# Kernel tuning notes

Measured on AMD Instinct MI355X. Metric: run time of the kernel, lower is better.

## Reference

```python
import jax, jax.numpy as jnp
import numpy as np

N = 100000
E = 1600000
IN_DIM = 128
HID = 64
HEADS = 4
OUT_DIM = 2
BN_EPS = 1e-5
NEG_SLOPE = 0.2


def setup_inputs() -> dict:
    key = jax.random.key(0)
    ks = jax.random.split(key, 16)
    inp = {
        "x": jax.random.normal(ks[0], (N, IN_DIM), jnp.float32),
        "edge_index": jax.random.randint(ks[1], (2, E), 0, N, jnp.int32),
        # layer 1: GATConv(IN_DIM, HID, heads=HEADS, concat=True)
        "W1": jax.random.normal(ks[2], (IN_DIM, HEADS * HID), jnp.float32) * 0.05,
        "att_src1": jax.random.normal(ks[3], (HEADS, HID), jnp.float32) * 0.05,
        "att_dst1": jax.random.normal(ks[4], (HEADS, HID), jnp.float32) * 0.05,
        "b1": jnp.zeros((HEADS * HID,), jnp.float32),
        # BatchNorm1d(HEADS*HID), eval mode (running stats)
        "gamma": jnp.ones((HEADS * HID,), jnp.float32),
        "beta": jnp.zeros((HEADS * HID,), jnp.float32),
        "rmean": jax.random.normal(ks[5], (HEADS * HID,), jnp.float32) * 0.01,
        "rvar": jnp.ones((HEADS * HID,), jnp.float32),
        # layer 2: GATConv(HEADS*HID, OUT_DIM, heads=1, concat=False)
        "W2": jax.random.normal(ks[6], (HEADS * HID, OUT_DIM), jnp.float32) * 0.05,
        "att_src2": jax.random.normal(ks[7], (1, OUT_DIM), jnp.float32) * 0.05,
        "att_dst2": jax.random.normal(ks[8], (1, OUT_DIM), jnp.float32) * 0.05,
        "b2": jnp.zeros((OUT_DIM,), jnp.float32),
    }
    return inp


def gat_conv(x, W, att_src, att_dst, src, dst):
    """PyG-style GATConv message passing. Returns [N, H, C] aggregated output."""
    H, C = att_src.shape
    h = (x @ W).reshape(-1, H, C)                      # [N,H,C]
    a_src = jnp.einsum('nhc,hc->nh', h, att_src)       # [N,H]
    a_dst = jnp.einsum('nhc,hc->nh', h, att_dst)       # [N,H]
    e = jax.nn.leaky_relu(a_src[src] + a_dst[dst], NEG_SLOPE)   # [E,H]
    # softmax over incoming edges per destination node (segment softmax)
    m = jax.ops.segment_max(e, dst, num_segments=h.shape[0])    # [N,H]
    ee = jnp.exp(e - m[dst])
    s = jax.ops.segment_sum(ee, dst, num_segments=h.shape[0])   # [N,H]
    alpha = ee / (s[dst] + 1e-16)                      # [E,H]
    msg = h[src] * alpha[:, :, None]                   # [E,H,C]
    return jax.ops.segment_sum(msg, dst, num_segments=h.shape[0])  # [N,H,C]


def reference(x, edge_index, W1, att_src1, att_dst1, b1,
              gamma, beta, rmean, rvar, W2, att_src2, att_dst2, b2):
    src, dst = edge_index[0], edge_index[1]
    # layer 1 (concat heads) + bias
    h = gat_conv(x, W1, att_src1, att_dst1, src, dst).reshape(N, HEADS * HID) + b1
    # BatchNorm1d (eval mode), ELU; dropout is identity in eval
    h = (h - rmean) * jax.lax.rsqrt(rvar + BN_EPS) * gamma + beta
    h = jax.nn.elu(h)
    # layer 2 (heads=1, concat=False -> mean over heads == squeeze) + bias
    out = gat_conv(h, W2, att_src2, att_dst2, src, dst).reshape(N, OUT_DIM) + b2
    return jax.nn.log_softmax(out, axis=1)
```

## Files before the change

kernel.cpp:

```cpp
#include <hip/hip_runtime.h>
#include <hip/hip_fp16.h>
#include <math.h>

#define NN 100000
#define EE 1600000
#define NEG 0.2f
#define NB 98
#define STRIP 128
#define GB 782
#define HB 6250

typedef _Float16 fh8 __attribute__((ext_vector_type(8)));
typedef float f32x4 __attribute__((ext_vector_type(4)));

__device__ __forceinline__ float lrelu(float v) { return v > 0.f ? v : NEG * v; }

__device__ __forceinline__ void fma8(const uint4& r, float w, float* acc)
{
    float2 f0 = __half22float2(*(const __half2*)&r.x);
    float2 f1 = __half22float2(*(const __half2*)&r.y);
    float2 f2 = __half22float2(*(const __half2*)&r.z);
    float2 f3 = __half22float2(*(const __half2*)&r.w);
    acc[0] = fmaf(w, f0.x, acc[0]); acc[1] = fmaf(w, f0.y, acc[1]);
    acc[2] = fmaf(w, f1.x, acc[2]); acc[3] = fmaf(w, f1.y, acc[3]);
    acc[4] = fmaf(w, f2.x, acc[4]); acc[5] = fmaf(w, f2.y, acc[5]);
    acc[6] = fmaf(w, f3.x, acc[6]); acc[7] = fmaf(w, f3.y, acc[7]);
}

__global__ __launch_bounds__(256) void prep_kernel(
    const float* __restrict__ W1,
    const float* __restrict__ b1, const float* __restrict__ gamma,
    const float* __restrict__ beta, const float* __restrict__ rmean,
    const float* __restrict__ rvar,
    _Float16* __restrict__ W1f, float* __restrict__ nA, float* __restrict__ nB,
    int* __restrict__ counts)
{
    int t = blockIdx.x * 256 + threadIdx.x;
    if (t < 64 * 64) {
        int l = t & 63, frag = t >> 6;
        int kk = frag & 3, ft = (frag >> 2) & 3, w = frag >> 4;
        int feat = w * 64 + ft * 16 + (l & 15);
        int kbase = kk * 32 + (l >> 4) * 8;
        _Float16 v[8];
#pragma unroll
        for (int i = 0; i < 8; i++) v[i] = (_Float16)W1[(size_t)(kbase + i) * 256 + feat];
        *(fh8*)&W1f[(size_t)t * 8] = *(fh8*)v;
    } else if (t < 64 * 64 + 256) {
        int f = t - 64 * 64;
        float scale = gamma[f] * rsqrtf(rvar[f] + 1e-5f);
        nA[f] = scale;
        nB[f] = (b1[f] - rmean[f]) * scale + beta[f];
    }
    for (int i = t; i < NN; i += 128 * 256) counts[i] = 0;
}

__global__ __launch_bounds__(256) void gemm1_hist(
    const float* __restrict__ x, const _Float16* __restrict__ W1f,
    const float* __restrict__ attS1, const float* __restrict__ attD1,
    __half* __restrict__ h1, float* __restrict__ asrc1, float* __restrict__ adst1,
    const int* __restrict__ ei, int* __restrict__ counts)
{
    const int bid = blockIdx.x;
    const int tid = threadIdx.x;
    if (bid >= GB) {
        int e = (bid - GB) * 256 + tid;
        if (e < EE) atomicAdd(&counts[ei[EE + e]], 1);
        return;
    }

    __shared__ _Float16 xh[STRIP][136];
    const int lane = tid & 63;
    const int w    = tid >> 6;
    const int base = bid * STRIP;

#pragma unroll
    for (int it = 0; it < 2; ++it) {
        int slot = tid + it * 256;
        int node = slot >> 2;
        int k0   = (slot & 3) * 32;
        int gnode = base + node;
        float4 buf[8];
        if (gnode < NN) {
            const float4* src = (const float4*)(x + (size_t)gnode * 128 + k0);
#pragma unroll
            for (int j = 0; j < 8; j++) buf[j] = src[j];
        } else {
#pragma unroll
            for (int j = 0; j < 8; j++) buf[j] = make_float4(0.f, 0.f, 0.f, 0.f);
        }
        _Float16* dst = &xh[node][k0];
#pragma unroll
        for (int j = 0; j < 8; j++) {
            dst[j * 4 + 0] = (_Float16)buf[j].x;
            dst[j * 4 + 1] = (_Float16)buf[j].y;
            dst[j * 4 + 2] = (_Float16)buf[j].z;
            dst[j * 4 + 3] = (_Float16)buf[j].w;
        }
    }
    __syncthreads();

    fh8 afrag[4][4];
    const fh8* wf = (const fh8*)W1f;
#pragma unroll
    for (int ft = 0; ft < 4; ft++)
#pragma unroll
        for (int kk = 0; kk < 4; kk++)
            afrag[ft][kk] = wf[((w * 4 + ft) * 4 + kk) * 64 + lane];

    const int nrow = lane & 15;
    const int kq   = lane >> 4;

    float attSv[4][4], attDv[4][4];
#pragma unroll
    for (int ft = 0; ft < 4; ft++)
#pragma unroll
        for (int r = 0; r < 4; r++) {
            int feat = w * 64 + ft * 16 + kq * 4 + r;
            attSv[ft][r] = attS1[feat];
            attDv[ft][r] = attD1[feat];
        }

    for (int g = 0; g < STRIP / 16; ++g) {
        fh8 b[4];
#pragma unroll
        for (int kk = 0; kk < 4; kk++)
            b[kk] = *(const fh8*)&xh[g * 16 + nrow][kk * 32 + kq * 8];

        f32x4 d[4];
#pragma unroll
        for (int ft = 0; ft < 4; ft++) {
            d[ft] = (f32x4){0.f, 0.f, 0.f, 0.f};
#pragma unroll
            for (int kk = 0; kk < 4; kk++)
                d[ft] = __builtin_amdgcn_mfma_f32_16x16x32_f16(afrag[ft][kk], b[kk], d[ft], 0, 0, 0);
        }

        int gnode = base + g * 16 + nrow;
        if (gnode < NN) {
            float ps = 0.f, pd = 0.f;
#pragma unroll
            for (int ft = 0; ft < 4; ft++) {
                __half hb[4];
#pragma unroll
                for (int r = 0; r < 4; r++) {
                    float v = d[ft][r];
                    hb[r] = __float2half(v);
                    ps = fmaf(v, attSv[ft][r], ps);
                    pd = fmaf(v, attDv[ft][r], pd);
                }
                *(float2*)&h1[(size_t)gnode * 256 + w * 64 + ft * 16 + kq * 4] = *(float2*)hb;
            }
            ps += __shfl_xor(ps, 16); ps += __shfl_xor(ps, 32);
            pd += __shfl_xor(pd, 16); pd += __shfl_xor(pd, 32);
            if (kq == 0) { asrc1[gnode * 4 + w] = ps; adst1[gnode * 4 + w] = pd; }
        }
    }
}

__global__ __launch_bounds__(256) void scan1_kernel(const int* __restrict__ counts, int* __restrict__ bsum)
{
    __shared__ int red[256];
    int t = threadIdx.x;
    int i0 = blockIdx.x * 1024 + t * 4;
    int s = 0;
    if (i0 + 3 < NN) {
        int4 v = *(const int4*)&counts[i0];
        s = v.x + v.y + v.z + v.w;
    } else {
#pragma unroll
        for (int j = 0; j < 4; j++) { int i = i0 + j; if (i < NN) s += counts[i]; }
    }
    red[t] = s;
    __syncthreads();
    for (int off = 128; off > 0; off >>= 1) {
        if (t < off) red[t] += red[t + off];
        __syncthreads();
    }
    if (t == 0) bsum[blockIdx.x] = red[0];
}

__global__ void scan2_kernel(const int* __restrict__ bsum, int* __restrict__ bbase, int* __restrict__ offs)
{
    __shared__ int sh[128];
    int t = threadIdx.x;
    int v = (t < NB) ? bsum[t] : 0;
    sh[t] = v;
    __syncthreads();
    for (int off = 1; off < 128; off <<= 1) {
        int u = (t >= off) ? sh[t - off] : 0;
        __syncthreads();
        sh[t] += u;
        __syncthreads();
    }
    if (t < NB) bbase[t] = sh[t] - v;
    if (t == 0) offs[NN] = EE;
}

__global__ __launch_bounds__(256) void scan3_kernel(const int* __restrict__ counts,
                                                    const int* __restrict__ bbase,
                                                    int* __restrict__ offs, int* __restrict__ cursor)
{
    __shared__ int sh[256];
    int t = threadIdx.x;
    int i0 = blockIdx.x * 1024 + t * 4;
    int c[4];
    int s = 0;
#pragma unroll
    for (int j = 0; j < 4; j++) { int i = i0 + j; c[j] = (i < NN) ? counts[i] : 0; s += c[j]; }
    sh[t] = s;
    __syncthreads();
    for (int off = 1; off < 256; off <<= 1) {
        int u = (t >= off) ? sh[t - off] : 0;
        __syncthreads();
        sh[t] += u;
        __syncthreads();
    }
    int run = bbase[blockIdx.x] + sh[t] - s;
    if (i0 + 3 < NN) {
        int4 o;
        o.x = run; run += c[0];
        o.y = run; run += c[1];
        o.z = run; run += c[2];
        o.w = run;
        *(int4*)&offs[i0] = o;
        *(int4*)&cursor[i0] = o;
    } else {
#pragma unroll
        for (int j = 0; j < 4; j++) { int i = i0 + j; if (i < NN) { offs[i] = run; cursor[i] = run; run += c[j]; } }
    }
}

__global__ void scatter_kernel(const int* __restrict__ ei,
                               const float* __restrict__ asrc1, const float* __restrict__ adst1,
                               int* __restrict__ cursor, int* __restrict__ csr_src,
                               float* __restrict__ ewp)
{
    int e = blockIdx.x * 256 + threadIdx.x;
    if (e >= EE) return;
    int s = ei[e], d = ei[EE + e];
    int pos = atomicAdd(&cursor[d], 1);
    csr_src[pos] = s;
    float4 as = *(const float4*)&asrc1[(size_t)s * 4];
    float4 ad = *(const float4*)&adst1[(size_t)d * 4];
    float4 w;
    w.x = expf(lrelu(as.x + ad.x));
    w.y = expf(lrelu(as.y + ad.y));
    w.z = expf(lrelu(as.z + ad.z));
    w.w = expf(lrelu(as.w + ad.w));
    *(float4*)&ewp[(size_t)pos * 4] = w;
}

__global__ __launch_bounds__(256) void agg1_kernel(
    const int* __restrict__ offs, const int* __restrict__ csr_src,
    const float* __restrict__ ewp, const __half* __restrict__ h1,
    float* __restrict__ g1)
{
    int wid  = (blockIdx.x * 256 + threadIdx.x) >> 6;
    int lane = threadIdx.x & 63;
    if (wid >= NN) return;
    int lo = offs[wid], hi = offs[wid + 1];
    const int ep   = lane >> 5;
    const int fl   = lane & 31;
    const int head = fl >> 3;

    float acc[8] = {0.f, 0.f, 0.f, 0.f, 0.f, 0.f, 0.f, 0.f};
    float wsum = 0.f;

    int base = lo;
    for (; base + 3 < hi; base += 4) {
        int idx0 = base + ep;
        int idx1 = base + 2 + ep;
        int s0 = csr_src[idx0];
        int s1 = csr_src[idx1];
        float w0 = ewp[(size_t)idx0 * 4 + head];
        float w1 = ewp[(size_t)idx1 * 4 + head];
        uint4 r0 = *(const uint4*)(h1 + (size_t)s0 * 256 + fl * 8);
        uint4 r1 = *(const uint4*)(h1 + (size_t)s1 * 256 + fl * 8);
        fma8(r0, w0, acc);
        fma8(r1, w1, acc);
        wsum += w0 + w1;
    }
    for (; base < hi; base += 2) {
        int idx = base + ep;
        float w = 0.f;
        uint4 r = make_uint4(0, 0, 0, 0);
        if (idx < hi) {
            int s = csr_src[idx];
            w = ewp[(size_t)idx * 4 + head];
            r = *(const uint4*)(h1 + (size_t)s * 256 + fl * 8);
        }
        fma8(r, w, acc);
        wsum += w;
    }

#pragma unroll
    for (int j = 0; j < 8; j++) acc[j] += __shfl_xor(acc[j], 32);
    wsum += __shfl_xor(wsum, 32);

    if (lane < 32) {
        float inv = 1.f / (wsum + 1e-16f);
        *(float4*)&g1[(size_t)wid * 256 + fl * 8]     = make_float4(acc[0] * inv, acc[1] * inv, acc[2] * inv, acc[3] * inv);
        *(float4*)&g1[(size_t)wid * 256 + fl * 8 + 4] = make_float4(acc[4] * inv, acc[5] * inv, acc[6] * inv, acc[7] * inv);
    }
}

__global__ __launch_bounds__(256) void node2_kernel(
    const float* __restrict__ g1,
    const float* __restrict__ nA, const float* __restrict__ nB,
    const float* __restrict__ W2, const float* __restrict__ attS2, const float* __restrict__ attD2,
    float4* __restrict__ pk2)
{
    int n    = blockIdx.x * 4 + (threadIdx.x >> 6);
    int lane = threadIdx.x & 63;
    if (n >= NN) return;
    int f4 = lane * 4;
    float4 v  = *(const float4*)&g1[(size_t)n * 256 + f4];
    float4 na = *(const float4*)&nA[f4];
    float4 nb = *(const float4*)&nB[f4];
    float va[4] = {v.x, v.y, v.z, v.w};
    float naa[4] = {na.x, na.y, na.z, na.w};
    float nba[4] = {nb.x, nb.y, nb.z, nb.w};
    float t[4];
#pragma unroll
    for (int j = 0; j < 4; j++) {
        float u = fmaf(va[j], naa[j], nba[j]);
        t[j] = u > 0.f ? u : expm1f(u);
    }
    float4 w01 = *(const float4*)&W2[(size_t)f4 * 2];
    float4 w23 = *(const float4*)&W2[(size_t)f4 * 2 + 4];
    float c0 = t[0] * w01.x + t[1] * w01.z + t[2] * w23.x + t[3] * w23.z;
    float c1 = t[0] * w01.y + t[1] * w01.w + t[2] * w23.y + t[3] * w23.w;
    for (int off = 1; off < 64; off <<= 1) {
        c0 += __shfl_xor(c0, off);
        c1 += __shfl_xor(c1, off);
    }
    if (lane == 0) {
        float as2 = c0 * attS2[0] + c1 * attS2[1];
        float ad2 = c0 * attD2[0] + c1 * attD2[1];
        pk2[n] = make_float4(as2, ad2, c0, c1);
    }
}

__global__ __launch_bounds__(256) void agg2_kernel(
    const int* __restrict__ offs, const int* __restrict__ csr_src,
    const float4* __restrict__ pk2, const float* __restrict__ b2,
    float* __restrict__ out)
{
    int wid  = (blockIdx.x * 256 + threadIdx.x) >> 6;
    int lane = threadIdx.x & 63;
    int grp  = lane >> 3;
    int sub  = lane & 7;
    int n = wid * 8 + grp;
    if (n >= NN) return;
    int lo = offs[n], hi = offs[n + 1];
    float ad = pk2[n].y;

    float n0 = 0.f, n1 = 0.f, ws = 0.f;
    for (int i = lo + sub; i < hi; i += 8) {
        int s = csr_src[i];
        float4 p = pk2[s];
        float w = expf(lrelu(p.x + ad));
        n0 = fmaf(w, p.z, n0);
        n1 = fmaf(w, p.w, n1);
        ws += w;
    }
    n0 += __shfl_xor(n0, 1); n0 += __shfl_xor(n0, 2); n0 += __shfl_xor(n0, 4);
    n1 += __shfl_xor(n1, 1); n1 += __shfl_xor(n1, 2); n1 += __shfl_xor(n1, 4);
    ws += __shfl_xor(ws, 1); ws += __shfl_xor(ws, 2); ws += __shfl_xor(ws, 4);

    if (sub == 0) {
        float inv = 1.f / (ws + 1e-16f);
        float v0 = n0 * inv + b2[0];
        float v1 = n1 * inv + b2[1];
        float m = fmaxf(v0, v1);
        float lse = m + log1pf(expf(fminf(v0, v1) - m));
        *(float2*)&out[(size_t)n * 2] = make_float2(v0 - lse, v1 - lse);
    }
}

extern "C" void kernel_launch(void* const* d_in, const int* in_sizes, int n_in,
                              void* d_out, int out_size, void* d_ws, size_t ws_size,
                              hipStream_t stream)
{
    const float* x     = (const float*)d_in[0];
    const int*   ei    = (const int*)d_in[1];
    const float* W1    = (const float*)d_in[2];
    const float* attS1 = (const float*)d_in[3];
    const float* attD1 = (const float*)d_in[4];
    const float* b1    = (const float*)d_in[5];
    const float* gamma = (const float*)d_in[6];
    const float* beta  = (const float*)d_in[7];
    const float* rmean = (const float*)d_in[8];
    const float* rvar  = (const float*)d_in[9];
    const float* W2    = (const float*)d_in[10];
    const float* attS2 = (const float*)d_in[11];
    const float* attD2 = (const float*)d_in[12];
    const float* b2    = (const float*)d_in[13];
    float* out = (float*)d_out;

    float* f = (float*)d_ws;
    __half* h1    = (__half*)f;
    float* asrc1  = f + (size_t)NN * 128;
    float* adst1  = asrc1 + (size_t)NN * 4;
    _Float16* W1f = (_Float16*)(adst1 + (size_t)NN * 4);
    float* nA     = adst1 + (size_t)NN * 4 + 16384;
    float* nB     = nA + 256;
    float4* pk2   = (float4*)(nB + 256);
    float* g1     = nB + 256 + (size_t)NN * 4;
    float* ewp    = g1 + (size_t)NN * 256;
    int* counts   = (int*)(ewp + (size_t)EE * 4);
    int* offs     = counts + NN;
    int* cursor   = offs + (NN + 1);
    int* bsum     = cursor + NN;
    int* bbase    = bsum + NB;
    int* csr_src  = bbase + NB;

    prep_kernel<<<128, 256, 0, stream>>>(W1, b1, gamma, beta, rmean, rvar, W1f, nA, nB, counts);

    gemm1_hist<<<GB + HB, 256, 0, stream>>>(x, W1f, attS1, attD1, h1, asrc1, adst1, ei, counts);

    scan1_kernel<<<NB, 256, 0, stream>>>(counts, bsum);
    scan2_kernel<<<1, 128, 0, stream>>>(bsum, bbase, offs);
    scan3_kernel<<<NB, 256, 0, stream>>>(counts, bbase, offs, cursor);

    scatter_kernel<<<HB, 256, 0, stream>>>(ei, asrc1, adst1, cursor, csr_src, ewp);

    agg1_kernel<<<(NN + 3) / 4, 256, 0, stream>>>(offs, csr_src, ewp, h1, g1);

    node2_kernel<<<(NN + 3) / 4, 256, 0, stream>>>(g1, nA, nB, W2, attS2, attD2, pk2);

    agg2_kernel<<<(NN + 31) / 32, 256, 0, stream>>>(offs, csr_src, pk2, b2, out);
}
```

Measured before the change: 344.5 us.

## Fuse node2 into agg1 and pack CSR source with fp16 edge weights

The layer-1 aggregation now feeds the BatchNorm, ELU and W2 projection straight from registers, so the 100000x256 float g1 buffer is never written and read back and one kernel launch goes away. The CSR source index and the four per-head exp weights are packed into a single 16-byte int4 record, with the weights stored as fp16, replacing separate csr_src and fp32 ewp arrays. This is meant to cut scatter and gather traffic. In exchange, edge weights lose precision, agg2 reads 16-byte records where it only needs the 4-byte index, and lanes 32-63 now do duplicate epilogue work.

```diff
diff --git a/kernel.cpp b/kernel.cpp
--- a/kernel.cpp
+++ b/kernel.cpp
@@ -25,6 +25,13 @@
     acc[2] = fmaf(w, f1.x, acc[2]); acc[3] = fmaf(w, f1.y, acc[3]);
     acc[4] = fmaf(w, f2.x, acc[4]); acc[5] = fmaf(w, f2.y, acc[5]);
     acc[6] = fmaf(w, f3.x, acc[6]); acc[7] = fmaf(w, f3.y, acc[7]);
+}
+
+__device__ __forceinline__ float ewgt(const int4& e, int head)
+{
+    uint p = (head < 2) ? (uint)e.y : (uint)e.z;
+    float2 f = __half22float2(*(const __half2*)&p);
+    return (head & 1) ? f.y : f.x;
 }
 
 __global__ __launch_bounds__(256) void prep_kernel(
@@ -232,28 +239,30 @@
 
 __global__ void scatter_kernel(const int* __restrict__ ei,
                                const float* __restrict__ asrc1, const float* __restrict__ adst1,
-                               int* __restrict__ cursor, int* __restrict__ csr_src,
-                               float* __restrict__ ewp)
+                               int* __restrict__ cursor, int4* __restrict__ csr)
 {
     int e = blockIdx.x * 256 + threadIdx.x;
     if (e >= EE) return;
     int s = ei[e], d = ei[EE + e];
     int pos = atomicAdd(&cursor[d], 1);
-    csr_src[pos] = s;
     float4 as = *(const float4*)&asrc1[(size_t)s * 4];
     float4 ad = *(const float4*)&adst1[(size_t)d * 4];
-    float4 w;
-    w.x = expf(lrelu(as.x + ad.x));
-    w.y = expf(lrelu(as.y + ad.y));
-    w.z = expf(lrelu(as.z + ad.z));
-    w.w = expf(lrelu(as.w + ad.w));
-    *(float4*)&ewp[(size_t)pos * 4] = w;
-}
-
-__global__ __launch_bounds__(256) void agg1_kernel(
-    const int* __restrict__ offs, const int* __restrict__ csr_src,
-    const float* __restrict__ ewp, const __half* __restrict__ h1,
-    float* __restrict__ g1)
+    __half2 w01 = __floats2half2_rn(expf(lrelu(as.x + ad.x)), expf(lrelu(as.y + ad.y)));
+    __half2 w23 = __floats2half2_rn(expf(lrelu(as.z + ad.z)), expf(lrelu(as.w + ad.w)));
+    int4 ent;
+    ent.x = s;
+    ent.y = *(const int*)&w01;
+    ent.z = *(const int*)&w23;
+    ent.w = 0;
+    csr[pos] = ent;
+}
+
+__global__ __launch_bounds__(256) void agg1_node2(
+    const int* __restrict__ offs, const int4* __restrict__ csr,
+    const __half* __restrict__ h1,
+    const float* __restrict__ nA, const float* __restrict__ nB,
+    const float* __restrict__ W2, const float* __restrict__ attS2, const float* __restrict__ attD2,
+    float4* __restrict__ pk2)
 {
     int wid  = (blockIdx.x * 256 + threadIdx.x) >> 6;
     int lane = threadIdx.x & 63;
@@ -270,12 +279,12 @@
     for (; base + 3 < hi; base += 4) {
         int idx0 = base + ep;
         int idx1 = base + 2 + ep;
-        int s0 = csr_src[idx0];
-        int s1 = csr_src[idx1];
-        float w0 = ewp[(size_t)idx0 * 4 + head];
-        float w1 = ewp[(size_t)idx1 * 4 + head];
-        uint4 r0 = *(const uint4*)(h1 + (size_t)s0 * 256 + fl * 8);
-        uint4 r1 = *(const uint4*)(h1 + (size_t)s1 * 256 + fl * 8);
+        int4 e0 = csr[idx0];
+        int4 e1 = csr[idx1];
+        float w0 = ewgt(e0, head);
+        float w1 = ewgt(e1, head);
+        uint4 r0 = *(const uint4*)(h1 + (size_t)e0.x * 256 + fl * 8);
+        uint4 r1 = *(const uint4*)(h1 + (size_t)e1.x * 256 + fl * 8);
         fma8(r0, w0, acc);
         fma8(r1, w1, acc);
         wsum += w0 + w1;
@@ -285,9 +294,9 @@
         float w = 0.f;
         uint4 r = make_uint4(0, 0, 0, 0);
         if (idx < hi) {
-            int s = csr_src[idx];
-            w = ewp[(size_t)idx * 4 + head];
-            r = *(const uint4*)(h1 + (size_t)s * 256 + fl * 8);
+            int4 e = csr[idx];
+            w = ewgt(e, head);
+            r = *(const uint4*)(h1 + (size_t)e.x * 256 + fl * 8);
         }
         fma8(r, w, acc);
         wsum += w;
@@ -297,52 +306,39 @@
     for (int j = 0; j < 8; j++) acc[j] += __shfl_xor(acc[j], 32);
     wsum += __shfl_xor(wsum, 32);
 
-    if (lane < 32) {
-        float inv = 1.f / (wsum + 1e-16f);
-        *(float4*)&g1[(size_t)wid * 256 + fl * 8]     = make_float4(acc[0] * inv, acc[1] * inv, acc[2] * inv, acc[3] * inv);
-        *(float4*)&g1[(size_t)wid * 256 + fl * 8 + 4] = make_float4(acc[4] * inv, acc[5] * inv, acc[6] * inv, acc[7] * inv);
-    }
-}
-
-__global__ __launch_bounds__(256) void node2_kernel(
-    const float* __restrict__ g1,
-    const float* __restrict__ nA, const float* __restrict__ nB,
-    const float* __restrict__ W2, const float* __restrict__ attS2, const float* __restrict__ attD2,
-    float4* __restrict__ pk2)
-{
-    int n    = blockIdx.x * 4 + (threadIdx.x >> 6);
-    int lane = threadIdx.x & 63;
-    if (n >= NN) return;
-    int f4 = lane * 4;
-    float4 v  = *(const float4*)&g1[(size_t)n * 256 + f4];
-    float4 na = *(const float4*)&nA[f4];
-    float4 nb = *(const float4*)&nB[f4];
-    float va[4] = {v.x, v.y, v.z, v.w};
-    float naa[4] = {na.x, na.y, na.z, na.w};
-    float nba[4] = {nb.x, nb.y, nb.z, nb.w};
-    float t[4];
-#pragma unroll
-    for (int j = 0; j < 4; j++) {
-        float u = fmaf(va[j], naa[j], nba[j]);
-        t[j] = u > 0.f ? u : expm1f(u);
-    }
-    float4 w01 = *(const float4*)&W2[(size_t)f4 * 2];
-    float4 w23 = *(const float4*)&W2[(size_t)f4 * 2 + 4];
-    float c0 = t[0] * w01.x + t[1] * w01.z + t[2] * w23.x + t[3] * w23.z;
-    float c1 = t[0] * w01.y + t[1] * w01.w + t[2] * w23.y + t[3] * w23.w;
-    for (int off = 1; off < 64; off <<= 1) {
-        c0 += __shfl_xor(c0, off);
-        c1 += __shfl_xor(c1, off);
-    }
+    float inv = 1.f / (wsum + 1e-16f);
+
+    float c0 = 0.f, c1 = 0.f;
+#pragma unroll
+    for (int half8 = 0; half8 < 2; ++half8) {
+        float4 na = *(const float4*)&nA[fl * 8 + half8 * 4];
+        float4 nb = *(const float4*)&nB[fl * 8 + half8 * 4];
+        float naa[4] = {na.x, na.y, na.z, na.w};
+        float nba[4] = {nb.x, nb.y, nb.z, nb.w};
+#pragma unroll
+        for (int j = 0; j < 4; j++) {
+            int f = fl * 8 + half8 * 4 + j;
+            float g = acc[half8 * 4 + j] * inv;
+            float u = fmaf(g, naa[j], nba[j]);
+            float t = u > 0.f ? u : expm1f(u);
+            c0 = fmaf(t, W2[f * 2],     c0);
+            c1 = fmaf(t, W2[f * 2 + 1], c1);
+        }
+    }
+    c0 += __shfl_xor(c0, 1); c0 += __shfl_xor(c0, 2); c0 += __shfl_xor(c0, 4);
+    c0 += __shfl_xor(c0, 8); c0 += __shfl_xor(c0, 16);
+    c1 += __shfl_xor(c1, 1); c1 += __shfl_xor(c1, 2); c1 += __shfl_xor(c1, 4);
+    c1 += __shfl_xor(c1, 8); c1 += __shfl_xor(c1, 16);
+
     if (lane == 0) {
         float as2 = c0 * attS2[0] + c1 * attS2[1];
         float ad2 = c0 * attD2[0] + c1 * attD2[1];
-        pk2[n] = make_float4(as2, ad2, c0, c1);
+        pk2[wid] = make_float4(as2, ad2, c0, c1);
     }
 }
 
 __global__ __launch_bounds__(256) void agg2_kernel(
-    const int* __restrict__ offs, const int* __restrict__ csr_src,
+    const int* __restrict__ offs, const int4* __restrict__ csr,
     const float4* __restrict__ pk2, const float* __restrict__ b2,
     float* __restrict__ out)
 {
@@ -357,7 +353,7 @@
 
     float n0 = 0.f, n1 = 0.f, ws = 0.f;
     for (int i = lo + sub; i < hi; i += 8) {
-        int s = csr_src[i];
+        int s = csr[i].x;
         float4 p = pk2[s];
         float w = expf(lrelu(p.x + ad));
         n0 = fmaf(w, p.z, n0);
@@ -406,14 +402,12 @@
     float* nA     = adst1 + (size_t)NN * 4 + 16384;
     float* nB     = nA + 256;
     float4* pk2   = (float4*)(nB + 256);
-    float* g1     = nB + 256 + (size_t)NN * 4;
-    float* ewp    = g1 + (size_t)NN * 256;
-    int* counts   = (int*)(ewp + (size_t)EE * 4);
+    int4* csr     = (int4*)(pk2 + NN);
+    int* counts   = (int*)(csr + EE);
     int* offs     = counts + NN;
     int* cursor   = offs + (NN + 1);
     int* bsum     = cursor + NN;
     int* bbase    = bsum + NB;
-    int* csr_src  = bbase + NB;
 
     prep_kernel<<<128, 256, 0, stream>>>(W1, b1, gamma, beta, rmean, rvar, W1f, nA, nB, counts);
 
@@ -423,11 +417,9 @@
     scan2_kernel<<<1, 128, 0, stream>>>(bsum, bbase, offs);
     scan3_kernel<<<NB, 256, 0, stream>>>(counts, bbase, offs, cursor);
 
-    scatter_kernel<<<HB, 256, 0, stream>>>(ei, asrc1, adst1, cursor, csr_src, ewp);
-
-    agg1_kernel<<<(NN + 3) / 4, 256, 0, stream>>>(offs, csr_src, ewp, h1, g1);
-
-    node2_kernel<<<(NN + 3) / 4, 256, 0, stream>>>(g1, nA, nB, W2, attS2, attD2, pk2);
-
-    agg2_kernel<<<(NN + 31) / 32, 256, 0, stream>>>(offs, csr_src, pk2, b2, out);
-}
+    scatter_kernel<<<HB, 256, 0, stream>>>(ei, asrc1, adst1, cursor, csr);
+
+    agg1_node2<<<(NN + 3) / 4, 256, 0, stream>>>(offs, csr, h1, nA, nB, W2, attS2, attD2, pk2);
+
+    agg2_kernel<<<(NN + 31) / 32, 256, 0, stream>>>(offs, csr, pk2, b2, out);
+}
```

Result: faster. 311.3 us (-9.6%).
